# Kernel optimization log

Measured on AMD Instinct MI355X. Metric: run time of the kernel, lower is better.

The kernel has to match this reference:

```python
import jax, jax.numpy as jnp
import numpy as np

V = 32000   # vocab
D = 1024    # dim
H = 16      # query heads
HKV = 8     # kv heads (GQA)
DH = D // H # head dim = 64
L = 2       # layers
FF = 3584   # expert hidden dim
E = 8       # experts
K = 2       # top-k
EPS = 1e-5
BASE = 1000000.0
B, S = 1, 2048


def setup_inputs() -> dict:
    key = jax.random.key(0)
    ks = jax.random.split(key, 10)
    s = 0.02
    return {
        "x": jax.random.randint(ks[0], (B, S), 0, V, dtype=jnp.int64) if jax.config.jax_enable_x64 else jax.random.randint(ks[0], (B, S), 0, V),
        "emb": jax.random.normal(ks[1], (V, D), jnp.float32) * s,
        "ln_w": jnp.ones((L, D), jnp.float32),
        "ffln_w": jnp.ones((L, D), jnp.float32),
        "wq": jax.random.normal(ks[2], (L, D, H * DH), jnp.float32) * s,
        "wk": jax.random.normal(ks[3], (L, D, HKV * DH), jnp.float32) * s,
        "wv": jax.random.normal(ks[4], (L, D, HKV * DH), jnp.float32) * s,
        "wo": jax.random.normal(ks[5], (L, H * DH, D), jnp.float32) * s,
        "gate_w": jax.random.normal(ks[6], (L, E, D), jnp.float32) * s,
        "w1": jax.random.normal(ks[7], (L, E, FF, D), jnp.float32) * s,
        "w2": jax.random.normal(ks[8], (L, E, D, FF), jnp.float32) * s,
        "w3": jax.random.normal(ks[9], (L, E, FF, D), jnp.float32) * s,
        "dec_norm_w": jnp.ones((D,), jnp.float32),
    }


def rmsnorm(x, w):
    # LayerNormParameterized(use_mean=False, shift=False) == RMSNorm, pow in fp32
    xf = x.astype(jnp.float32)
    var = jnp.mean(xf * xf, axis=-1, keepdims=True)
    return ((xf * jax.lax.rsqrt(var + EPS)).astype(x.dtype)) * w


def rope(xh, pos):
    # interleaved (complex-pair) rotary embedding, xh: [B, S, h, DH]
    half = DH // 2
    freqs = 1.0 / (BASE ** (jnp.arange(0, half, dtype=jnp.float32) * 2.0 / DH))
    ang = pos[:, None] * freqs[None, :]                       # [S, half]
    cos = jnp.cos(ang)[None, :, None, :]
    sin = jnp.sin(ang)[None, :, None, :]
    x1 = xh[..., 0::2]
    x2 = xh[..., 1::2]
    out = jnp.stack([x1 * cos - x2 * sin, x1 * sin + x2 * cos], axis=-1)
    return out.reshape(xh.shape)


def reference(x, emb, ln_w, ffln_w, wq, wk, wv, wo, gate_w, w1, w2, w3, dec_norm_w):
    h = emb[x]                                                # [B, S, D]
    pos = jnp.arange(S, dtype=jnp.float32)
    causal = jnp.tril(jnp.ones((S, S), bool))[None, None]     # [1,1,S,S]
    scale = 1.0 / np.sqrt(DH).astype(np.float32)
    for i in range(L):
        # --- attention sub-layer ---
        res = h
        xn = rmsnorm(h, ln_w[i])
        q = rope((xn @ wq[i]).reshape(B, S, H, DH), pos)
        k = rope((xn @ wk[i]).reshape(B, S, HKV, DH), pos)
        v = (xn @ wv[i]).reshape(B, S, HKV, DH)
        rep = H // HKV
        k = jnp.repeat(k, rep, axis=2)                        # [B,S,H,DH]
        v = jnp.repeat(v, rep, axis=2)
        scores = jnp.einsum('bqhd,bkhd->bhqk', q, k) * scale
        scores = jnp.where(causal, scores, jnp.float32(-1e9))
        att = jax.nn.softmax(scores, axis=-1)
        o = jnp.einsum('bhqk,bkhd->bqhd', att, v).reshape(B, S, H * DH) @ wo[i]
        h = res + o
        # --- MoE FFN sub-layer ---
        res = h
        xn = rmsnorm(h, ffln_w[i]).reshape(B * S, D)          # [T, D]
        logits = xn @ gate_w[i].T                             # [T, E]
        gates = jax.nn.softmax(logits, axis=-1)
        topw, topi = jax.lax.top_k(gates, K)                  # [T, K]
        topw = topw / jnp.sum(topw, axis=-1, keepdims=True)
        # dense combine weights [T, E] (zero for unselected experts)
        cw = jnp.einsum('tk,tke->te', topw, jax.nn.one_hot(topi, E, dtype=topw.dtype))
        y = jnp.zeros_like(xn)
        for e in range(E):                                    # fixed small expert loop
            ye = (jax.nn.silu(xn @ w1[i, e].T) * (xn @ w3[i, e].T)) @ w2[i, e].T
            y = y + cw[:, e:e + 1] * ye
        h = res + y.reshape(B, S, D)
    return rmsnorm(h, dec_norm_w)
```

## Files before the change

kernel.cpp:

```cpp
#include <hip/hip_runtime.h>

using u16 = unsigned short;
using u32 = unsigned int;

#define TT 2048
#define DM 1024
#define NH 16
#define NKV 8
#define DHD 64
#define FFD 3584
#define NE 8

typedef __bf16 bf16x8 __attribute__((ext_vector_type(8)));
typedef float f32x4 __attribute__((ext_vector_type(4)));

__device__ __forceinline__ u16 f2bf(float x){
  return __builtin_bit_cast(u16, (__bf16)x);
}
__device__ __forceinline__ float bf2f(u16 h){
  return (float)__builtin_bit_cast(__bf16, h);
}
__device__ __forceinline__ f32x4 mfma16(bf16x8 a, bf16x8 b, f32x4 c){
  return __builtin_amdgcn_mfma_f32_16x16x32_bf16(a, b, c, 0, 0, 0);
}
__device__ __forceinline__ uint4 packhi8v(float4 a, float4 b){
  u16 h0=f2bf(a.x),h1=f2bf(a.y),h2=f2bf(a.z),h3=f2bf(a.w);
  u16 h4=f2bf(b.x),h5=f2bf(b.y),h6=f2bf(b.z),h7=f2bf(b.w);
  return make_uint4((u32)h0|((u32)h1<<16),(u32)h2|((u32)h3<<16),
                    (u32)h4|((u32)h5<<16),(u32)h6|((u32)h7<<16));
}
__device__ __forceinline__ uint4 packlo8v(float4 a, float4 b){
  u16 l0=f2bf(a.x-bf2f(f2bf(a.x))),l1=f2bf(a.y-bf2f(f2bf(a.y)));
  u16 l2=f2bf(a.z-bf2f(f2bf(a.z))),l3=f2bf(a.w-bf2f(f2bf(a.w)));
  u16 l4=f2bf(b.x-bf2f(f2bf(b.x))),l5=f2bf(b.y-bf2f(f2bf(b.y)));
  u16 l6=f2bf(b.z-bf2f(f2bf(b.z))),l7=f2bf(b.w-bf2f(f2bf(b.w)));
  return make_uint4((u32)l0|((u32)l1<<16),(u32)l2|((u32)l3<<16),
                    (u32)l4|((u32)l5<<16),(u32)l6|((u32)l7<<16));
}

__global__ __launch_bounds__(256) void k_embed(const int* __restrict__ x,
    const float* __restrict__ emb, float* __restrict__ h){
  int t = blockIdx.x;
  int d = threadIdx.x * 4;
  float4 v = *reinterpret_cast<const float4*>(emb + (size_t)x[t] * DM + d);
  *reinterpret_cast<float4*>(h + (size_t)t * DM + d) = v;
}

template<int OUTF32>
__global__ __launch_bounds__(256) void k_rmsnorm(const float* __restrict__ in,
    const float* __restrict__ w, u16* __restrict__ oh, u16* __restrict__ ol,
    float* __restrict__ of){
  int t = blockIdx.x;
  int d4 = threadIdx.x * 4;
  float4 xv = *reinterpret_cast<const float4*>(in + (size_t)t * DM + d4);
  float ss = xv.x*xv.x + xv.y*xv.y + xv.z*xv.z + xv.w*xv.w;
#pragma unroll
  for (int m = 1; m < 64; m <<= 1) ss += __shfl_xor(ss, m);
  __shared__ float sred[4];
  if ((threadIdx.x & 63) == 0) sred[threadIdx.x >> 6] = ss;
  __syncthreads();
  float tot = sred[0] + sred[1] + sred[2] + sred[3];
  float r = 1.0f / sqrtf(tot * (1.0f / DM) + 1e-5f);
  float vv[4] = {xv.x, xv.y, xv.z, xv.w};
#pragma unroll
  for (int jj = 0; jj < 4; jj++){
    float xn = (vv[jj] * r) * w[d4 + jj];
    size_t a = (size_t)t * DM + d4 + jj;
    if constexpr (OUTF32){
      of[a] = xn;
    } else {
      u16 hi = f2bf(xn);
      oh[a] = hi;
      ol[a] = f2bf(xn - bf2f(hi));
    }
  }
}

template<int NHD>
__global__ __launch_bounds__(256) void k_rope(const float* __restrict__ in,
    u16* __restrict__ oh, u16* __restrict__ ol){
  int idx = blockIdx.x * 256 + threadIdx.x;
  int j = idx & 31;
  int hd = (idx >> 5) % NHD;
  int s = idx / (32 * NHD);
  size_t base = ((size_t)s * NHD + hd) * 64 + 2 * j;
  float x1 = in[base], x2 = in[base + 1];
  float xe = (float)j * 0.03125f;
  float yf = (float)pow(1.0e6, (double)xe);
  float fr = 1.0f / yf;
  float ang = (float)s * fr;
  double ad = (double)ang;
  float c  = (float)cos(ad);
  float sn = (float)sin(ad);
  float o1 = x1 * c - x2 * sn;
  float o2 = x1 * sn + x2 * c;
  u16 h1 = f2bf(o1), h2 = f2bf(o2);
  oh[base]     = h1; ol[base]     = f2bf(o1 - bf2f(h1));
  oh[base + 1] = h2; ol[base + 1] = f2bf(o2 - bf2f(h2));
}

__global__ __launch_bounds__(256) void k_splitbuf(const float* __restrict__ in,
    u16* __restrict__ oh, u16* __restrict__ ol, int n){
  int i = blockIdx.x * 256 + threadIdx.x;
  if (i < n){
    float x = in[i];
    u16 hi = f2bf(x);
    oh[i] = hi;
    ol[i] = f2bf(x - bf2f(hi));
  }
}

__global__ __launch_bounds__(256) void k_gate(const u16* __restrict__ xh,
    const u16* __restrict__ xl, const float* __restrict__ gw,
    int* __restrict__ topi, float* __restrict__ topw, int* __restrict__ cnt){
  int wv = threadIdx.x >> 6, lane = threadIdx.x & 63;
  int t = blockIdx.x * 4 + wv;
  float x[16];
#pragma unroll
  for (int i = 0; i < 16; i++){
    size_t a = (size_t)t * DM + lane + 64 * i;
    x[i] = bf2f(xh[a]) + bf2f(xl[a]);
  }
  float lgt[8];
#pragma unroll
  for (int e = 0; e < 8; e++){
    float s = 0.f;
#pragma unroll
    for (int i = 0; i < 16; i++) s += x[i] * gw[(size_t)e * DM + lane + 64 * i];
#pragma unroll
    for (int m = 1; m < 64; m <<= 1) s += __shfl_xor(s, m);
    lgt[e] = s;
  }
  float mx = lgt[0];
#pragma unroll
  for (int e = 1; e < 8; e++) mx = fmaxf(mx, lgt[e]);
  float p[8]; float sum = 0.f;
#pragma unroll
  for (int e = 0; e < 8; e++){ p[e] = expf(lgt[e] - mx); sum += p[e]; }
  float g[8];
#pragma unroll
  for (int e = 0; e < 8; e++) g[e] = p[e] / sum;
  int t0 = 0; float b0 = g[0];
#pragma unroll
  for (int e = 1; e < 8; e++) if (g[e] > b0){ b0 = g[e]; t0 = e; }
  int t1 = -1; float b1 = -1.f;
#pragma unroll
  for (int e = 0; e < 8; e++) if (e != t0 && g[e] > b1){ b1 = g[e]; t1 = e; }
  float ssum = b0 + b1;
  float w0 = b0 / ssum, w1 = b1 / ssum;
  if (lane == 0 && t < TT){
    topi[2*t] = t0; topi[2*t+1] = t1;
    topw[2*t] = w0; topw[2*t+1] = w1;
    atomicAdd(&cnt[t0], 1);
    atomicAdd(&cnt[t1], 1);
  }
}

__global__ void k_zero8(int* cnt){ if (threadIdx.x < 8) cnt[threadIdx.x] = 0; }

__global__ void k_scan(const int* __restrict__ cnt, int* __restrict__ offp, int* __restrict__ cur){
  if (threadIdx.x == 0){
    int r = 0;
    for (int e = 0; e < 8; e++){ offp[e] = r; r += cnt[e]; }
  }
  if (threadIdx.x < 8) cur[threadIdx.x] = 0;
}

__global__ __launch_bounds__(256) void k_scatter(const int* __restrict__ topi,
    const float* __restrict__ topw, const int* __restrict__ offp, int* __restrict__ cur,
    int* __restrict__ ftok, float* __restrict__ fwt){
  int t = blockIdx.x * 256 + threadIdx.x;
  if (t < TT){
#pragma unroll
    for (int j = 0; j < 2; j++){
      int e = topi[2*t + j];
      int p = atomicAdd(&cur[e], 1);
      ftok[offp[e] + p] = t;
      fwt[offp[e] + p] = topw[2*t + j];
    }
  }
}

#define GPRELOAD(KK) do { \
    pAh0 = *reinterpret_cast<const uint4*>(Ah + arowA + (KK)); \
    pAh1 = *reinterpret_cast<const uint4*>(Ah + arowA + (KK) + 8); \
    if constexpr (SPLIT){ \
      pAl0 = *reinterpret_cast<const uint4*>(Al + arowA + (KK)); \
      pAl1 = *reinterpret_cast<const uint4*>(Al + arowA + (KK) + 8); \
    } \
    if constexpr (BLAYOUT == 0){ \
      const float* bp_ = Bw + (size_t)(n0 + bn) * K + (KK) + bc; \
      pB0 = *reinterpret_cast<const float4*>(bp_); \
      pB1 = *reinterpret_cast<const float4*>(bp_ + 4); \
      if constexpr (TN == 128){ \
        pB2 = *reinterpret_cast<const float4*>(bp_ + 8); \
        pB3 = *reinterpret_cast<const float4*>(bp_ + 12); \
      } \
      if constexpr (DUAL){ \
        const float* bq_ = B3w + (size_t)(n0 + bn) * K + (KK) + bc; \
        pB2 = *reinterpret_cast<const float4*>(bq_); \
        pB3 = *reinterpret_cast<const float4*>(bq_ + 4); \
      } \
    } else { \
      pB0 = *reinterpret_cast<const float4*>(Bw + (size_t)((KK) + kk1) * Nq + n0 + nn1); \
      pB1 = *reinterpret_cast<const float4*>(Bw + (size_t)((KK) + 16 + kk1) * Nq + n0 + nn1); \
    } \
  } while(0)

template<int BLAYOUT, int EPI, int SPLIT, int DUAL, int TN, int KS>
__global__ __launch_bounds__(256) void k_gemm(
    const u16* __restrict__ Ah, const u16* __restrict__ Al,
    const float* __restrict__ Bw, const float* __restrict__ B3w,
    const float* __restrict__ Bw2, const float* __restrict__ Bw3,
    size_t strideB, int N, int K,
    float* __restrict__ Cf, int ldc,
    float* __restrict__ Cf2, float* __restrict__ Cf3,
    u16* __restrict__ Ch, u16* __restrict__ Cl,
    const int* __restrict__ cntp, const int* __restrict__ offp,
    const int* __restrict__ ftok, const float* __restrict__ fwt)
{
  static_assert(!(DUAL && TN != 64), "DUAL uses TN=64");
  static_assert(!(BLAYOUT == 1 && TN != 64), "BLAYOUT=1 uses TN=64");
  int cnt = TT, off = 0, ks = 0;
  if constexpr (EPI == 2 || EPI == 3){
    int e = blockIdx.z / KS;
    ks = blockIdx.z % KS;
    cnt = cntp[e]; off = offp[e];
    if ((int)blockIdx.y * 128 >= cnt) return;
    Bw += (size_t)e * strideB;
    if constexpr (DUAL) B3w += (size_t)e * strideB;
  } else if constexpr (KS > 1){
    ks = blockIdx.z;
  }
  __shared__ u16 Ash[128][42];
  __shared__ u16 Asl[SPLIT ? 128 : 1][42];
  __shared__ u16 Bh1[TN][42];
  __shared__ u16 Bl1[SPLIT ? TN : 1][42];
  __shared__ u16 Bh3[DUAL ? TN : 1][42];
  __shared__ u16 Bl3[(DUAL && SPLIT) ? TN : 1][42];

  const int tid = threadIdx.x;
  const int m0 = blockIdx.y * 128;

  int n0, Nq = N, ldq = ldc;
  float* Cq = Cf;
  if constexpr (EPI == 4){
    int bx = blockIdx.x;
    if (bx < 16){       n0 = bx * 64;        Nq = 1024; ldq = 1024; Cq = Cf;  }
    else if (bx < 24){  n0 = (bx - 16) * 64; Nq = 512;  ldq = 512;  Cq = Cf2; Bw = Bw2; }
    else {              n0 = (bx - 24) * 64; Nq = 512;  ldq = 512;  Cq = Cf3; Bw = Bw3; }
  } else {
    n0 = blockIdx.x * TN;
  }

  const int ar = tid >> 1;
  const int ac = (tid & 1) * 16;
  int gidx = m0 + ar;
  int gr;
  if constexpr (EPI == 2){
    int ii = gidx < cnt ? gidx : cnt - 1;
    gr = ftok[off + ii];
  } else if constexpr (EPI == 3){
    gr = off + (gidx < cnt ? gidx : cnt - 1);
  } else {
    gr = gidx;
  }
  const size_t arowA = (size_t)gr * K + ac;

  const int bn  = (TN == 128) ? (tid >> 1) : (tid >> 2);
  const int bc  = (TN == 128) ? ((tid & 1) * 16) : ((tid & 3) * 8);
  const int kk1 = tid >> 4;
  const int nn1 = (tid & 15) * 4;

  const int wid = tid >> 6, lane = tid & 63;
  const int wr = wid >> 1, wc = wid & 1;
  const int lr = lane & 15, lg = lane >> 4;
  constexpr int NF = TN / 32;

  f32x4 acc[4][NF];
  f32x4 acc3[DUAL ? 4 : 1][NF];
#pragma unroll
  for (int m = 0; m < 4; m++)
#pragma unroll
    for (int n = 0; n < NF; n++){
      acc[m][n] = f32x4{0.f,0.f,0.f,0.f};
      if constexpr (DUAL) acc3[m][n] = f32x4{0.f,0.f,0.f,0.f};
    }

  uint4 pAh0, pAh1, pAl0{}, pAl1{};
  float4 pB0{}, pB1{}, pB2{}, pB3{};

  const int kbeg = ks * (K / KS);
  const int kend = kbeg + (K / KS);

  GPRELOAD(kbeg);
  for (int k0 = kbeg; k0 < kend; k0 += 32){
    *reinterpret_cast<uint4*>(&Ash[ar][ac]) = pAh0;
    *reinterpret_cast<uint4*>(&Ash[ar][ac + 8]) = pAh1;
    if constexpr (SPLIT){
      *reinterpret_cast<uint4*>(&Asl[ar][ac]) = pAl0;
      *reinterpret_cast<uint4*>(&Asl[ar][ac + 8]) = pAl1;
    }
    if constexpr (BLAYOUT == 0){
      *reinterpret_cast<uint4*>(&Bh1[bn][bc]) = packhi8v(pB0, pB1);
      if constexpr (SPLIT) *reinterpret_cast<uint4*>(&Bl1[bn][bc]) = packlo8v(pB0, pB1);
      if constexpr (TN == 128){
        *reinterpret_cast<uint4*>(&Bh1[bn][bc + 8]) = packhi8v(pB2, pB3);
        if constexpr (SPLIT) *reinterpret_cast<uint4*>(&Bl1[bn][bc + 8]) = packlo8v(pB2, pB3);
      }
      if constexpr (DUAL){
        *reinterpret_cast<uint4*>(&Bh3[bn][bc]) = packhi8v(pB2, pB3);
        if constexpr (SPLIT) *reinterpret_cast<uint4*>(&Bl3[bn][bc]) = packlo8v(pB2, pB3);
      }
    } else {
      const float* q0 = reinterpret_cast<const float*>(&pB0);
      const float* q1 = reinterpret_cast<const float*>(&pB1);
#pragma unroll
      for (int j = 0; j < 4; j++){
        u16 h0 = f2bf(q0[j]);
        Bh1[nn1 + j][kk1] = h0;
        if constexpr (SPLIT) Bl1[nn1 + j][kk1] = f2bf(q0[j] - bf2f(h0));
        u16 h1 = f2bf(q1[j]);
        Bh1[nn1 + j][kk1 + 16] = h1;
        if constexpr (SPLIT) Bl1[nn1 + j][kk1 + 16] = f2bf(q1[j] - bf2f(h1));
      }
    }
    __syncthreads();
    if (k0 + 32 < kend){ GPRELOAD(k0 + 32); }

    bf16x8 af[4], afl[4];
#pragma unroll
    for (int m = 0; m < 4; m++){
      af[m] = *reinterpret_cast<const bf16x8*>(&Ash[wr*64 + m*16 + lr][lg*8]);
      if constexpr (SPLIT)
        afl[m] = *reinterpret_cast<const bf16x8*>(&Asl[wr*64 + m*16 + lr][lg*8]);
    }
#pragma unroll
    for (int n = 0; n < NF; n++){
      int col = wc*(TN/2) + n*16 + lr;
      bf16x8 b1 = *reinterpret_cast<const bf16x8*>(&Bh1[col][lg*8]);
#pragma unroll
      for (int m = 0; m < 4; m++) acc[m][n] = mfma16(af[m], b1, acc[m][n]);
      if constexpr (SPLIT){
        bf16x8 bl = *reinterpret_cast<const bf16x8*>(&Bl1[col][lg*8]);
#pragma unroll
        for (int m = 0; m < 4; m++){
          acc[m][n] = mfma16(af[m], bl, acc[m][n]);
          acc[m][n] = mfma16(afl[m], b1, acc[m][n]);
        }
      }
      if constexpr (DUAL){
        bf16x8 b3 = *reinterpret_cast<const bf16x8*>(&Bh3[col][lg*8]);
#pragma unroll
        for (int m = 0; m < 4; m++) acc3[m][n] = mfma16(af[m], b3, acc3[m][n]);
        if constexpr (SPLIT){
          bf16x8 b3l = *reinterpret_cast<const bf16x8*>(&Bl3[col][lg*8]);
#pragma unroll
          for (int m = 0; m < 4; m++){
            acc3[m][n] = mfma16(af[m], b3l, acc3[m][n]);
            acc3[m][n] = mfma16(afl[m], b3, acc3[m][n]);
          }
        }
      }
    }
    __syncthreads();
  }

#pragma unroll
  for (int m = 0; m < 4; m++)
#pragma unroll
    for (int n = 0; n < NF; n++)
#pragma unroll
      for (int r = 0; r < 4; r++){
        int row = m0 + wr*64 + m*16 + lg*4 + r;
        int col = n0 + wc*(TN/2) + n*16 + lr;
        float v = acc[m][n][r];
        if constexpr (EPI == 0){
          Cf[(size_t)row * ldc + col] = v;
        } else if constexpr (EPI == 1){
          if constexpr (KS > 1) atomicAdd(&Cf[(size_t)row * ldc + col], v);
          else                  Cf[(size_t)row * ldc + col] += v;
        } else if constexpr (EPI == 2){
          if (row < cnt){
            float a3 = acc3[m][n][r];
            float s = v / (1.0f + expf(-v));
            float y = s * a3;
            u16 hi = f2bf(y);
            size_t oa = (size_t)(off + row) * ldc + col;
            Ch[oa] = hi;
            Cl[oa] = f2bf(y - bf2f(hi));
          }
        } else if constexpr (EPI == 3){
          if (row < cnt){
            int tok = ftok[off + row];
            float wgt = fwt[off + row];
            atomicAdd(&Cf[(size_t)tok * ldc + col], wgt * v);
          }
        } else {
          if constexpr (KS > 1) atomicAdd(&Cq[(size_t)row * ldq + col], v);
          else                  Cq[(size_t)row * ldq + col] = v;
        }
      }
}

__global__ __launch_bounds__(256) void k_attn(
    const u16* __restrict__ qh, const u16* __restrict__ ql,
    const u16* __restrict__ kh, const u16* __restrict__ kl,
    const u16* __restrict__ vh, const u16* __restrict__ vl,
    u16* __restrict__ aoh, u16* __restrict__ aol)
{
  const int h  = blockIdx.y;
  const int q0 = blockIdx.x * 64;
  const int hk = h >> 1;
  const int tid = threadIdx.x;
  const int wv = tid >> 6, lane = tid & 63;
  const int lr = lane & 15, lg = lane >> 4;
  const int qw0 = q0 + wv * 16;

  __shared__ u16 Khs[32][74], Kls[32][74];
  __shared__ u16 Vhs[64][42], Vls[64][42];
  __shared__ u16 Phs[4][16][42], Pls[4][16][42];

  bf16x8 qfh[2], qfl[2];
#pragma unroll
  for (int dc = 0; dc < 2; dc++){
    size_t qa = ((size_t)(qw0 + lr) * NH + h) * 64 + dc*32 + lg*8;
    qfh[dc] = *reinterpret_cast<const bf16x8*>(qh + qa);
    qfl[dc] = *reinterpret_cast<const bf16x8*>(ql + qa);
  }
  f32x4 oacc[4];
  float mrun[4], lrun[4];
#pragma unroll
  for (int r = 0; r < 4; r++){ mrun[r] = -1e30f; lrun[r] = 0.f; }
#pragma unroll
  for (int g = 0; g < 4; g++) oacc[g] = f32x4{0.f,0.f,0.f,0.f};

  const int nt = q0 / 32 + 2;
  for (int kt = 0; kt < nt; kt++){
    int kg = kt * 32;
    {
      int kk = tid >> 3, c8 = (tid & 7) * 8;
      size_t ka = ((size_t)(kg + kk) * NKV + hk) * 64 + c8;
      *reinterpret_cast<uint4*>(&Khs[kk][c8]) = *reinterpret_cast<const uint4*>(kh + ka);
      *reinterpret_cast<uint4*>(&Kls[kk][c8]) = *reinterpret_cast<const uint4*>(kl + ka);
      uint4 v1 = *reinterpret_cast<const uint4*>(vh + ka);
      uint4 v2 = *reinterpret_cast<const uint4*>(vl + ka);
      const u16* p1 = reinterpret_cast<const u16*>(&v1);
      const u16* p2 = reinterpret_cast<const u16*>(&v2);
#pragma unroll
      for (int j = 0; j < 8; j++){ Vhs[c8 + j][kk] = p1[j]; Vls[c8 + j][kk] = p2[j]; }
    }
    __syncthreads();

    f32x4 sc[2];
    sc[0] = f32x4{0.f,0.f,0.f,0.f};
    sc[1] = f32x4{0.f,0.f,0.f,0.f};
#pragma unroll
    for (int c = 0; c < 2; c++){
#pragma unroll
      for (int dc = 0; dc < 2; dc++){
        bf16x8 bh = *reinterpret_cast<const bf16x8*>(&Khs[c*16 + lr][dc*32 + lg*8]);
        bf16x8 bl = *reinterpret_cast<const bf16x8*>(&Kls[c*16 + lr][dc*32 + lg*8]);
        sc[c] = mfma16(qfh[dc], bh, sc[c]);
        sc[c] = mfma16(qfh[dc], bl, sc[c]);
        sc[c] = mfma16(qfl[dc], bh, sc[c]);
      }
    }
    float pnew[2][4], corr[4];
#pragma unroll
    for (int r = 0; r < 4; r++){
      int row = qw0 + lg*4 + r;
      float s0 = (kg + lr      <= row) ? sc[0][r] * 0.125f : -1e30f;
      float s1 = (kg + 16 + lr <= row) ? sc[1][r] * 0.125f : -1e30f;
      float tm = fmaxf(s0, s1);
#pragma unroll
      for (int m = 1; m < 16; m <<= 1) tm = fmaxf(tm, __shfl_xor(tm, m));
      float mnew = fmaxf(mrun[r], tm);
      corr[r] = expf(mrun[r] - mnew);
      float p0 = expf(s0 - mnew);
      float p1 = expf(s1 - mnew);
      pnew[0][r] = p0; pnew[1][r] = p1;
      float sm = p0 + p1;
#pragma unroll
      for (int m = 1; m < 16; m <<= 1) sm += __shfl_xor(sm, m);
      lrun[r] = lrun[r] * corr[r] + sm;
      mrun[r] = mnew;
    }
#pragma unroll
    for (int g = 0; g < 4; g++){
      f32x4 t = oacc[g];
#pragma unroll
      for (int r = 0; r < 4; r++) t[r] *= corr[r];
      oacc[g] = t;
    }
#pragma unroll
    for (int c = 0; c < 2; c++)
#pragma unroll
      for (int r = 0; r < 4; r++){
        float p = pnew[c][r];
        u16 hi = f2bf(p);
        Phs[wv][lg*4 + r][c*16 + lr] = hi;
        Pls[wv][lg*4 + r][c*16 + lr] = f2bf(p - bf2f(hi));
      }
    asm volatile("s_waitcnt lgkmcnt(0)" ::: "memory");
    __builtin_amdgcn_sched_barrier(0);
    bf16x8 pah = *reinterpret_cast<const bf16x8*>(&Phs[wv][lr][lg*8]);
    bf16x8 pal = *reinterpret_cast<const bf16x8*>(&Pls[wv][lr][lg*8]);
#pragma unroll
    for (int g = 0; g < 4; g++){
      bf16x8 vb1 = *reinterpret_cast<const bf16x8*>(&Vhs[g*16 + lr][lg*8]);
      bf16x8 vb2 = *reinterpret_cast<const bf16x8*>(&Vls[g*16 + lr][lg*8]);
      oacc[g] = mfma16(pah, vb1, oacc[g]);
      oacc[g] = mfma16(pah, vb2, oacc[g]);
      oacc[g] = mfma16(pal, vb1, oacc[g]);
    }
    __syncthreads();
  }
#pragma unroll
  for (int g = 0; g < 4; g++)
#pragma unroll
    for (int r = 0; r < 4; r++){
      int row = qw0 + lg*4 + r;
      float v = oacc[g][r] / lrun[r];
      u16 hi = f2bf(v);
      size_t oa = ((size_t)row * NH + h) * 64 + g*16 + lr;
      aoh[oa] = hi;
      aol[oa] = f2bf(v - bf2f(hi));
    }
}

extern "C" void kernel_launch(void* const* d_in, const int* in_sizes, int n_in,
                              void* d_out, int out_size, void* d_ws, size_t ws_size,
                              hipStream_t stream){
  const int*   x     = (const int*)d_in[0];
  const float* emb   = (const float*)d_in[1];
  const float* lnw   = (const float*)d_in[2];
  const float* fflnw = (const float*)d_in[3];
  const float* wq    = (const float*)d_in[4];
  const float* wk    = (const float*)d_in[5];
  const float* wvp   = (const float*)d_in[6];
  const float* wo    = (const float*)d_in[7];
  const float* gw    = (const float*)d_in[8];
  const float* w1    = (const float*)d_in[9];
  const float* w2    = (const float*)d_in[10];
  const float* w3    = (const float*)d_in[11];
  const float* dnw   = (const float*)d_in[12];
  float* out = (float*)d_out;

  char* p = (char*)d_ws;
  auto alloc = [&](size_t bytes)->char*{
    char* r = p; p += (bytes + 255) & ~(size_t)255; return r;
  };
  float* h    = (float*)alloc((size_t)TT * DM * 4);
  float* qbuf = (float*)alloc((size_t)TT * 1024 * 4);
  float* kbuf = (float*)alloc((size_t)TT * 512 * 4);
  float* vbuf = (float*)alloc((size_t)TT * 512 * 4);
  u16* xnh = (u16*)alloc((size_t)TT * DM * 2);
  u16* xnl = (u16*)alloc((size_t)TT * DM * 2);
  u16* qhb = (u16*)alloc((size_t)TT * 1024 * 2);
  u16* qlb = (u16*)alloc((size_t)TT * 1024 * 2);
  u16* khb = (u16*)alloc((size_t)TT * 512 * 2);
  u16* klb = (u16*)alloc((size_t)TT * 512 * 2);
  u16* vhb = (u16*)alloc((size_t)TT * 512 * 2);
  u16* vlb = (u16*)alloc((size_t)TT * 512 * 2);
  u16* aoh = (u16*)alloc((size_t)TT * 1024 * 2);
  u16* aol = (u16*)alloc((size_t)TT * 1024 * 2);
  u16* acth = (u16*)alloc((size_t)2 * TT * FFD * 2);
  u16* actl = (u16*)alloc((size_t)2 * TT * FFD * 2);
  int*   topi = (int*)alloc((size_t)2 * TT * 4);
  float* topw = (float*)alloc((size_t)2 * TT * 4);
  int* cnt  = (int*)alloc(64);
  int* offe = (int*)alloc(64);
  int* cur  = (int*)alloc(64);
  int*   ftok = (int*)alloc((size_t)2 * TT * 4);
  float* fwt  = (float*)alloc((size_t)2 * TT * 4);

  k_embed<<<TT, 256, 0, stream>>>(x, emb, h);

  for (int i = 0; i < 2; i++){
    const float* wq_i = wq + (size_t)i * DM * 1024;
    const float* wk_i = wk + (size_t)i * DM * 512;
    const float* wv_i = wvp + (size_t)i * DM * 512;
    const float* wo_i = wo + (size_t)i * 1024 * DM;
    const float* w1_i = w1 + (size_t)i * NE * FFD * DM;
    const float* w2_i = w2 + (size_t)i * NE * DM * FFD;
    const float* w3_i = w3 + (size_t)i * NE * FFD * DM;

    k_rmsnorm<0><<<TT, 256, 0, stream>>>(h, lnw + i * DM, xnh, xnl, nullptr);

    hipMemsetAsync(qbuf, 0, (size_t)TT * 1024 * 4, stream);
    hipMemsetAsync(kbuf, 0, (size_t)TT * 512 * 4, stream);
    hipMemsetAsync(vbuf, 0, (size_t)TT * 512 * 4, stream);
    k_gemm<1,4,1,0,64,2><<<dim3(32,16,2), 256, 0, stream>>>(xnh, xnl,
        wq_i, nullptr, wk_i, wv_i, 0, 1024, DM,
        qbuf, 1024, kbuf, vbuf, nullptr, nullptr, nullptr, nullptr, nullptr, nullptr);

    k_rope<16><<<4096, 256, 0, stream>>>(qbuf, qhb, qlb);
    k_rope<8><<<2048, 256, 0, stream>>>(kbuf, khb, klb);
    k_splitbuf<<<4096, 256, 0, stream>>>(vbuf, vhb, vlb, TT * 512);

    k_attn<<<dim3(32,16,1), 256, 0, stream>>>(qhb, qlb, khb, klb, vhb, vlb, aoh, aol);

    k_gemm<1,1,1,0,64,2><<<dim3(16,16,2), 256, 0, stream>>>(aoh, aol,
        wo_i, nullptr, nullptr, nullptr, 0, DM, 1024,
        h, DM, nullptr, nullptr, nullptr, nullptr, nullptr, nullptr, nullptr, nullptr);

    k_rmsnorm<0><<<TT, 256, 0, stream>>>(h, fflnw + i * DM, xnh, xnl, nullptr);

    k_zero8<<<1, 64, 0, stream>>>(cnt);
    k_gate<<<TT/4, 256, 0, stream>>>(xnh, xnl, gw + (size_t)i * NE * DM, topi, topw, cnt);
    k_scan<<<1, 64, 0, stream>>>(cnt, offe, cur);
    k_scatter<<<8, 256, 0, stream>>>(topi, topw, offe, cur, ftok, fwt);

    if (i == 0){
      k_gemm<0,2,1,1,64,1><<<dim3(FFD/64,16,8), 256, 0, stream>>>(xnh, xnl,
          w1_i, w3_i, nullptr, nullptr, (size_t)FFD * DM, FFD, DM,
          nullptr, FFD, nullptr, nullptr, acth, actl, cnt, offe, ftok, fwt);
      k_gemm<0,3,1,0,128,4><<<dim3(DM/128,16,32), 256, 0, stream>>>(acth, actl,
          w2_i, nullptr, nullptr, nullptr, (size_t)DM * FFD, DM, FFD,
          h, DM, nullptr, nullptr, nullptr, nullptr, cnt, offe, ftok, fwt);
    } else {
      k_gemm<0,2,0,1,64,1><<<dim3(FFD/64,16,8), 256, 0, stream>>>(xnh, xnl,
          w1_i, w3_i, nullptr, nullptr, (size_t)FFD * DM, FFD, DM,
          nullptr, FFD, nullptr, nullptr, acth, actl, cnt, offe, ftok, fwt);
      k_gemm<0,3,0,0,128,4><<<dim3(DM/128,16,32), 256, 0, stream>>>(acth, actl,
          w2_i, nullptr, nullptr, nullptr, (size_t)DM * FFD, DM, FFD,
          h, DM, nullptr, nullptr, nullptr, nullptr, cnt, offe, ftok, fwt);
    }
  }

  k_rmsnorm<1><<<TT, 256, 0, stream>>>(h, dnw, nullptr, nullptr, out);
}
```

Baseline: 1.631 ms.

## Swizzle GEMM shared-memory tiles and tighten attention LDS padding

Replaces the padded 42-element LDS rows in the GEMM with unpadded 32-element rows and an XOR swizzle on 8-element chunks. It also remaps the global-to-LDS load assignment so each thread loads one 8-wide chunk from two rows, 64 rows apart. The aim is aligned 16-byte LDS accesses without bank conflicts on the MFMA fragment reads, plus less LDS per block. The attention kernel's padding is shrunk to multiples of 8, which makes the vector accesses aligned but could add bank conflicts there.

```diff
diff --git a/kernel.cpp b/kernel.cpp
--- a/kernel.cpp
+++ b/kernel.cpp
@@ -37,6 +37,8 @@
   return make_uint4((u32)l0|((u32)l1<<16),(u32)l2|((u32)l3<<16),
                     (u32)l4|((u32)l5<<16),(u32)l6|((u32)l7<<16));
 }
+
+#define SWC(r,c) ((((c) ^ ((((r)>>1) ^ ((r)>>3)) & 3))) * 8)
 
 __global__ __launch_bounds__(256) void k_embed(const int* __restrict__ x,
     const float* __restrict__ emb, float* __restrict__ h){
@@ -182,22 +184,23 @@
 }
 
 #define GPRELOAD(KK) do { \
-    pAh0 = *reinterpret_cast<const uint4*>(Ah + arowA + (KK)); \
-    pAh1 = *reinterpret_cast<const uint4*>(Ah + arowA + (KK) + 8); \
+    pAh0 = *reinterpret_cast<const uint4*>(Ah + arowA0 + (KK)); \
+    pAh1 = *reinterpret_cast<const uint4*>(Ah + arowA1 + (KK)); \
     if constexpr (SPLIT){ \
-      pAl0 = *reinterpret_cast<const uint4*>(Al + arowA + (KK)); \
-      pAl1 = *reinterpret_cast<const uint4*>(Al + arowA + (KK) + 8); \
+      pAl0 = *reinterpret_cast<const uint4*>(Al + arowA0 + (KK)); \
+      pAl1 = *reinterpret_cast<const uint4*>(Al + arowA1 + (KK)); \
     } \
     if constexpr (BLAYOUT == 0){ \
-      const float* bp_ = Bw + (size_t)(n0 + bn) * K + (KK) + bc; \
+      const float* bp_ = Bw + (size_t)(n0 + br0) * K + (KK) + cb8; \
       pB0 = *reinterpret_cast<const float4*>(bp_); \
       pB1 = *reinterpret_cast<const float4*>(bp_ + 4); \
       if constexpr (TN == 128){ \
-        pB2 = *reinterpret_cast<const float4*>(bp_ + 8); \
-        pB3 = *reinterpret_cast<const float4*>(bp_ + 12); \
+        const float* bp2_ = Bw + (size_t)(n0 + br1) * K + (KK) + cb8; \
+        pB2 = *reinterpret_cast<const float4*>(bp2_); \
+        pB3 = *reinterpret_cast<const float4*>(bp2_ + 4); \
       } \
       if constexpr (DUAL){ \
-        const float* bq_ = B3w + (size_t)(n0 + bn) * K + (KK) + bc; \
+        const float* bq_ = B3w + (size_t)(n0 + br0) * K + (KK) + cb8; \
         pB2 = *reinterpret_cast<const float4*>(bq_); \
         pB3 = *reinterpret_cast<const float4*>(bq_ + 4); \
       } \
@@ -232,12 +235,12 @@
   } else if constexpr (KS > 1){
     ks = blockIdx.z;
   }
-  __shared__ u16 Ash[128][42];
-  __shared__ u16 Asl[SPLIT ? 128 : 1][42];
-  __shared__ u16 Bh1[TN][42];
-  __shared__ u16 Bl1[SPLIT ? TN : 1][42];
-  __shared__ u16 Bh3[DUAL ? TN : 1][42];
-  __shared__ u16 Bl3[(DUAL && SPLIT) ? TN : 1][42];
+  __shared__ u16 Ash[128][32];
+  __shared__ u16 Asl[SPLIT ? 128 : 1][32];
+  __shared__ u16 Bh1[TN][32];
+  __shared__ u16 Bl1[SPLIT ? TN : 1][32];
+  __shared__ u16 Bh3[DUAL ? TN : 1][32];
+  __shared__ u16 Bl3[(DUAL && SPLIT) ? TN : 1][32];
 
   const int tid = threadIdx.x;
   const int m0 = blockIdx.y * 128;
@@ -253,22 +256,31 @@
     n0 = blockIdx.x * TN;
   }
 
-  const int ar = tid >> 1;
-  const int ac = (tid & 1) * 16;
-  int gidx = m0 + ar;
-  int gr;
-  if constexpr (EPI == 2){
-    int ii = gidx < cnt ? gidx : cnt - 1;
-    gr = ftok[off + ii];
-  } else if constexpr (EPI == 3){
-    gr = off + (gidx < cnt ? gidx : cnt - 1);
-  } else {
-    gr = gidx;
-  }
-  const size_t arowA = (size_t)gr * K + ac;
-
-  const int bn  = (TN == 128) ? (tid >> 1) : (tid >> 2);
-  const int bc  = (TN == 128) ? ((tid & 1) * 16) : ((tid & 3) * 8);
+  const int r0 = tid >> 2;
+  const int r1 = r0 + 64;
+  const int ca = tid & 3;
+  const int ca8 = ca * 8;
+  int gr0, gr1;
+  {
+    int g0 = m0 + r0, g1 = m0 + r1;
+    if constexpr (EPI == 2){
+      gr0 = ftok[off + (g0 < cnt ? g0 : cnt - 1)];
+      gr1 = ftok[off + (g1 < cnt ? g1 : cnt - 1)];
+    } else if constexpr (EPI == 3){
+      gr0 = off + (g0 < cnt ? g0 : cnt - 1);
+      gr1 = off + (g1 < cnt ? g1 : cnt - 1);
+    } else {
+      gr0 = g0; gr1 = g1;
+    }
+  }
+  const size_t arowA0 = (size_t)gr0 * K + ca8;
+  const size_t arowA1 = (size_t)gr1 * K + ca8;
+  const int swA0 = SWC(r0, ca), swA1 = SWC(r1, ca);
+
+  const int br0 = tid >> 2;
+  const int br1 = br0 + 64;
+  const int cb8 = (tid & 3) * 8;
+  const int swB0 = SWC(br0, tid & 3), swB1 = SWC(br1, tid & 3);
   const int kk1 = tid >> 4;
   const int nn1 = (tid & 15) * 4;
 
@@ -295,34 +307,38 @@
 
   GPRELOAD(kbeg);
   for (int k0 = kbeg; k0 < kend; k0 += 32){
-    *reinterpret_cast<uint4*>(&Ash[ar][ac]) = pAh0;
-    *reinterpret_cast<uint4*>(&Ash[ar][ac + 8]) = pAh1;
+    *reinterpret_cast<uint4*>(&Ash[r0][swA0]) = pAh0;
+    *reinterpret_cast<uint4*>(&Ash[r1][swA1]) = pAh1;
     if constexpr (SPLIT){
-      *reinterpret_cast<uint4*>(&Asl[ar][ac]) = pAl0;
-      *reinterpret_cast<uint4*>(&Asl[ar][ac + 8]) = pAl1;
+      *reinterpret_cast<uint4*>(&Asl[r0][swA0]) = pAl0;
+      *reinterpret_cast<uint4*>(&Asl[r1][swA1]) = pAl1;
     }
     if constexpr (BLAYOUT == 0){
-      *reinterpret_cast<uint4*>(&Bh1[bn][bc]) = packhi8v(pB0, pB1);
-      if constexpr (SPLIT) *reinterpret_cast<uint4*>(&Bl1[bn][bc]) = packlo8v(pB0, pB1);
+      *reinterpret_cast<uint4*>(&Bh1[br0][swB0]) = packhi8v(pB0, pB1);
+      if constexpr (SPLIT) *reinterpret_cast<uint4*>(&Bl1[br0][swB0]) = packlo8v(pB0, pB1);
       if constexpr (TN == 128){
-        *reinterpret_cast<uint4*>(&Bh1[bn][bc + 8]) = packhi8v(pB2, pB3);
-        if constexpr (SPLIT) *reinterpret_cast<uint4*>(&Bl1[bn][bc + 8]) = packlo8v(pB2, pB3);
+        *reinterpret_cast<uint4*>(&Bh1[br1][swB1]) = packhi8v(pB2, pB3);
+        if constexpr (SPLIT) *reinterpret_cast<uint4*>(&Bl1[br1][swB1]) = packlo8v(pB2, pB3);
       }
       if constexpr (DUAL){
-        *reinterpret_cast<uint4*>(&Bh3[bn][bc]) = packhi8v(pB2, pB3);
-        if constexpr (SPLIT) *reinterpret_cast<uint4*>(&Bl3[bn][bc]) = packlo8v(pB2, pB3);
+        *reinterpret_cast<uint4*>(&Bh3[br0][swB0]) = packhi8v(pB2, pB3);
+        if constexpr (SPLIT) *reinterpret_cast<uint4*>(&Bl3[br0][swB0]) = packlo8v(pB2, pB3);
       }
     } else {
       const float* q0 = reinterpret_cast<const float*>(&pB0);
       const float* q1 = reinterpret_cast<const float*>(&pB1);
+      const int ch0 = kk1 >> 3, off0 = kk1 & 7;
 #pragma unroll
       for (int j = 0; j < 4; j++){
+        int row = nn1 + j;
+        int c0 = SWC(row, ch0) + off0;
+        int c1 = SWC(row, ch0 + 2) + off0;
         u16 h0 = f2bf(q0[j]);
-        Bh1[nn1 + j][kk1] = h0;
-        if constexpr (SPLIT) Bl1[nn1 + j][kk1] = f2bf(q0[j] - bf2f(h0));
+        Bh1[row][c0] = h0;
+        if constexpr (SPLIT) Bl1[row][c0] = f2bf(q0[j] - bf2f(h0));
         u16 h1 = f2bf(q1[j]);
-        Bh1[nn1 + j][kk1 + 16] = h1;
-        if constexpr (SPLIT) Bl1[nn1 + j][kk1 + 16] = f2bf(q1[j] - bf2f(h1));
+        Bh1[row][c1] = h1;
+        if constexpr (SPLIT) Bl1[row][c1] = f2bf(q1[j] - bf2f(h1));
       }
     }
     __syncthreads();
@@ -331,18 +347,21 @@
     bf16x8 af[4], afl[4];
 #pragma unroll
     for (int m = 0; m < 4; m++){
-      af[m] = *reinterpret_cast<const bf16x8*>(&Ash[wr*64 + m*16 + lr][lg*8]);
+      int Ra = wr*64 + m*16 + lr;
+      int sa = SWC(Ra, lg);
+      af[m] = *reinterpret_cast<const bf16x8*>(&Ash[Ra][sa]);
       if constexpr (SPLIT)
-        afl[m] = *reinterpret_cast<const bf16x8*>(&Asl[wr*64 + m*16 + lr][lg*8]);
+        afl[m] = *reinterpret_cast<const bf16x8*>(&Asl[Ra][sa]);
     }
 #pragma unroll
     for (int n = 0; n < NF; n++){
-      int col = wc*(TN/2) + n*16 + lr;
-      bf16x8 b1 = *reinterpret_cast<const bf16x8*>(&Bh1[col][lg*8]);
+      int Rb = wc*(TN/2) + n*16 + lr;
+      int sb = SWC(Rb, lg);
+      bf16x8 b1 = *reinterpret_cast<const bf16x8*>(&Bh1[Rb][sb]);
 #pragma unroll
       for (int m = 0; m < 4; m++) acc[m][n] = mfma16(af[m], b1, acc[m][n]);
       if constexpr (SPLIT){
-        bf16x8 bl = *reinterpret_cast<const bf16x8*>(&Bl1[col][lg*8]);
+        bf16x8 bl = *reinterpret_cast<const bf16x8*>(&Bl1[Rb][sb]);
 #pragma unroll
         for (int m = 0; m < 4; m++){
           acc[m][n] = mfma16(af[m], bl, acc[m][n]);
@@ -350,11 +369,11 @@
         }
       }
       if constexpr (DUAL){
-        bf16x8 b3 = *reinterpret_cast<const bf16x8*>(&Bh3[col][lg*8]);
+        bf16x8 b3 = *reinterpret_cast<const bf16x8*>(&Bh3[Rb][sb]);
 #pragma unroll
         for (int m = 0; m < 4; m++) acc3[m][n] = mfma16(af[m], b3, acc3[m][n]);
         if constexpr (SPLIT){
-          bf16x8 b3l = *reinterpret_cast<const bf16x8*>(&Bl3[col][lg*8]);
+          bf16x8 b3l = *reinterpret_cast<const bf16x8*>(&Bl3[Rb][sb]);
 #pragma unroll
           for (int m = 0; m < 4; m++){
             acc3[m][n] = mfma16(af[m], b3l, acc3[m][n]);
@@ -417,9 +436,9 @@
   const int lr = lane & 15, lg = lane >> 4;
   const int qw0 = q0 + wv * 16;
 
-  __shared__ u16 Khs[32][74], Kls[32][74];
-  __shared__ u16 Vhs[64][42], Vls[64][42];
-  __shared__ u16 Phs[4][16][42], Pls[4][16][42];
+  __shared__ u16 Khs[32][72], Kls[32][72];
+  __shared__ u16 Vhs[64][40], Vls[64][40];
+  __shared__ u16 Phs[4][16][40], Pls[4][16][40];
 
   bf16x8 qfh[2], qfl[2];
 #pragma unroll
```

Measured after the change: 1.530 ms. 1.07x faster.
